# Optimization experiments

Hardware: AMD Instinct MI355X
Metric: run time of the kernel (lower is better)

Reference implementation:

```python
import jax, jax.numpy as jnp
import numpy as np

V, B, L, NG = 50000, 128, 350, 3        # vocab, batch(docs), doc length, n-gram window
D, H, C = 768, 256, 20                  # bert dim, num_hidden, class_num
HEADS, LAYERS, K, ALPHA = 8, 2, 3, 0.15 # GAT heads/layers, diffusion hops k, alpha


def setup_inputs() -> dict:
    rng = np.random.default_rng(0)
    # per-doc graphs: 350 unique word-ids per doc (nodes), n-gram window edges
    node_ids = np.stack([rng.choice(V, L, replace=False) for _ in range(B)]).ravel()
    src_b, dst_b = [], []
    for i in range(L):
        for j in range(max(0, i - NG), min(L, i + NG + 1)):
            src_b.append(i); dst_b.append(j)
    src_b, dst_b = np.asarray(src_b), np.asarray(dst_b)
    off = (np.arange(B) * L)[:, None]
    edge_src = (src_b[None, :] + off).ravel()
    edge_dst = (dst_b[None, :] + off).ravel()
    graph_id = np.repeat(np.arange(B), L)

    ks = jax.random.split(jax.random.key(0), 8)
    f32 = jnp.float32
    return {
        'node_ids': jnp.asarray(node_ids, jnp.int32),
        'edge_src': jnp.asarray(edge_src, jnp.int32),
        'edge_dst': jnp.asarray(edge_dst, jnp.int32),
        'graph_id': jnp.asarray(graph_id, jnp.int32),
        'emb':    (jax.random.normal(ks[0], (V, D), f32) * 0.02),
        'W1':     (jax.random.normal(ks[1], (D, H), f32) / np.sqrt(D)).astype(f32),
        'b1':     jnp.zeros((H,), f32),
        'W2':     (jax.random.normal(ks[2], (H, C), f32) / np.sqrt(H)).astype(f32),
        'b2':     jnp.zeros((C,), f32),
        'gat_W':  (jax.random.normal(ks[3], (LAYERS, HEADS, C, C), f32) / np.sqrt(C)).astype(f32),
        'a_src':  (jax.random.normal(ks[4], (LAYERS, HEADS, C), f32) * 0.1),
        'a_dst':  (jax.random.normal(ks[5], (LAYERS, HEADS, C), f32) * 0.1),
        'w_gate': (jax.random.normal(ks[6], (C,), f32) / np.sqrt(C)).astype(f32),
        'b_gate': jnp.zeros((), f32),
    }


def _gat_layer(h, W, a_s, a_d, src, dst, N):
    # h: [N,C]; W: [Hd,C,C]; a_s/a_d: [Hd,C]
    z = jnp.einsum('nc,hcd->hnd', h, W)                     # [Hd,N,C]
    e = jax.nn.leaky_relu(jnp.einsum('hnd,hd->hn', z, a_s)[:, src]
                          + jnp.einsum('hnd,hd->hn', z, a_d)[:, dst], 0.2)  # [Hd,E]

    def segsoftmax(ev):  # edge softmax over incoming edges at each dst node
        m = jax.ops.segment_max(ev, dst, num_segments=N)
        ex = jnp.exp(ev - m[dst])
        s = jax.ops.segment_sum(ex, dst, num_segments=N)
        return ex / (s[dst] + 1e-9)

    att = jax.vmap(segsoftmax)(e)                           # [Hd,E]

    def diffuse(zh, ah):  # attention diffusion: Z_t = (1-a) A Z_{t-1} + a Z_0
        zt = zh
        for _ in range(K):
            agg = jax.ops.segment_sum(ah[:, None] * zt[src], dst, num_segments=N)
            zt = (1.0 - ALPHA) * agg + ALPHA * zh
        return zt

    out = jax.vmap(diffuse)(z, att)                         # [Hd,N,C]
    return jax.nn.elu(out).mean(axis=0)                     # merge='mean'


def reference(node_ids, edge_src, edge_dst, graph_id, emb, W1, b1, W2, b2,
              gat_W, a_src, a_dst, w_gate, b_gate):
    N = node_ids.shape[0]
    x = emb[node_ids]                                       # [N,768] gather
    x = jax.nn.relu(x @ W1 + b1)                            # linear1 + ReLU
    h = x @ W2 + b2                                         # linear2 -> [N,C]
    for l in range(LAYERS):
        h = _gat_layer(h, gat_W[l], a_src[l], a_dst[l], edge_src, edge_dst, N)
    gate = jax.nn.sigmoid(h @ w_gate + b_gate)[:, None]     # WeightAndSum gate
    return jax.ops.segment_sum(gate * h, graph_id, num_segments=B)  # [B,C]
```

## Files before the change

kernel.cpp:

```cpp
#include <hip/hip_runtime.h>
#include <hip/hip_bf16.h>
#include <cstddef>

#define NB_NODES 44800
#define NDOCS 128
#define DLEN 350
#define DIM 768
#define HID 256
#define NCLS 20
#define NHEADS 8
#define ZSTR 24

typedef __bf16 v8bf __attribute__((ext_vector_type(8)));
typedef __bf16 v4bf __attribute__((ext_vector_type(4)));
typedef float v4f __attribute__((ext_vector_type(4)));

__global__ __launch_bounds__(256) void k_transpose(const float* __restrict__ W1,
                                                   __bf16* __restrict__ W1T) {
  int idx = blockIdx.x * 256 + threadIdx.x;
  int n = idx / 768, k = idx - n * 768;
  W1T[idx] = (__bf16)W1[k * 256 + n];
}

__global__ __launch_bounds__(256) void k_mlp(
    const int* __restrict__ node_ids, const float* __restrict__ emb,
    const __bf16* __restrict__ W1T, const float* __restrict__ b1,
    const float* __restrict__ W2, const float* __restrict__ b2,
    float* __restrict__ h0) {
  __shared__ __align__(16) char smem[43520];
  __bf16* As = (__bf16*)smem;
  float*  xs = (float*)smem;
  __bf16* w2s = (__bf16*)(smem + 33280);
  int tid = threadIdx.x;
  int wave = tid >> 6, lane = tid & 63;
  int quad = lane >> 4, l16 = lane & 15;
  int m0 = blockIdx.x * 64;

  int lrow = tid & 15;
  int lk4  = (tid >> 4) & 3;
  int khalf = (tid >> 6) & 1;
  int msubA = tid >> 7;
  int kbase = khalf * 32 + lk4 * 8;
  const float* apA = emb + (size_t)node_ids[m0 + msubA * 16 + lrow] * DIM + kbase;
  const float* apB = emb + (size_t)node_ids[m0 + (msubA + 2) * 16 + lrow] * DIM + kbase;

  v4f acc[4][4];
#pragma unroll
  for (int ms = 0; ms < 4; ++ms)
#pragma unroll
    for (int j = 0; j < 4; ++j) acc[ms][j] = (v4f){0.f, 0.f, 0.f, 0.f};

  v4f pf[4];
  pf[0] = *(const v4f*)(apA); pf[1] = *(const v4f*)(apA + 4);
  pf[2] = *(const v4f*)(apB); pf[3] = *(const v4f*)(apB + 4);

  for (int kc = 0; kc < 12; ++kc) {
    __bf16* buf = As + (kc & 1) * 4096;
    v8bf w0, w1;
#pragma unroll
    for (int e = 0; e < 4; ++e) {
      w0[e] = (__bf16)pf[0][e]; w0[4 + e] = (__bf16)pf[1][e];
      w1[e] = (__bf16)pf[2][e]; w1[4 + e] = (__bf16)pf[3][e];
    }
    *(v8bf*)(buf + tid * 8) = w0;
    *(v8bf*)(buf + tid * 8 + 2048) = w1;
    if (kc < 11) {
      int k1 = (kc + 1) * 64;
      pf[0] = *(const v4f*)(apA + k1); pf[1] = *(const v4f*)(apA + k1 + 4);
      pf[2] = *(const v4f*)(apB + k1); pf[3] = *(const v4f*)(apB + k1 + 4);
    }
    __syncthreads();

#pragma unroll
    for (int ks = 0; ks < 2; ++ks) {
      v8bf af[4], bv[4];
#pragma unroll
      for (int ms = 0; ms < 4; ++ms)
        af[ms] = *(const v8bf*)(buf + ((ms * 2 + ks) * 64 + lane) * 8);
#pragma unroll
      for (int j = 0; j < 4; ++j)
        bv[j] = *(const v8bf*)(W1T + (size_t)(wave * 64 + j * 16 + l16) * DIM + kc * 64 + ks * 32 + quad * 8);
#pragma unroll
      for (int ms = 0; ms < 4; ++ms)
#pragma unroll
        for (int j = 0; j < 4; ++j)
          acc[ms][j] = __builtin_amdgcn_mfma_f32_16x16x32_bf16(af[ms], bv[j], acc[ms][j], 0, 0, 0);
    }
  }

  __syncthreads();
  for (int i = tid; i < HID * NCLS; i += 256) w2s[i] = (__bf16)W2[i];

#pragma unroll
  for (int p = 0; p < 2; ++p) {
    if (p) __syncthreads();
#pragma unroll
    for (int mh = 0; mh < 2; ++mh) {
      int ms = p * 2 + mh;
#pragma unroll
      for (int j = 0; j < 4; ++j) {
        int col = wave * 64 + j * 16 + l16;
        float bb = b1[col];
#pragma unroll
        for (int r = 0; r < 4; ++r) {
          int lr = mh * 16 + quad * 4 + r;
          float v = acc[ms][j][r] + bb;
          xs[lr * 260 + col] = v > 0.f ? v : 0.f;
        }
      }
    }
    __syncthreads();
    if (tid < 160) {
      int m = tid / 5, c0 = (tid % 5) * 4;
      v4f s = *(const v4f*)(b2 + c0);
      for (int k = 0; k < HID; ++k) {
        float x = xs[m * 260 + k];
        v4bf w = *(const v4bf*)(w2s + k * NCLS + c0);
        s[0] += x * (float)w[0]; s[1] += x * (float)w[1];
        s[2] += x * (float)w[2]; s[3] += x * (float)w[3];
      }
      *(v4f*)(h0 + (size_t)(m0 + p * 32 + m) * NCLS + c0) = s;
    }
  }
}

__global__ __launch_bounds__(384) void k_gat(
    const float* __restrict__ hin, const float* __restrict__ gatW,
    const float* __restrict__ a_src, const float* __restrict__ a_dst,
    int layer, float* __restrict__ zout) {
  __shared__ float zA[DLEN * ZSTR];
  __shared__ float asv[DLEN], adv[DLEN];
  int tid = threadIdx.x;
  int head = blockIdx.x & 7;
  int doc = blockIdx.x >> 3;
  const float* W  = gatW  + (size_t)(layer * NHEADS + head) * NCLS * NCLS;
  const float* av = a_src + (layer * NHEADS + head) * NCLS;
  const float* dv = a_dst + (layer * NHEADS + head) * NCLS;
  int r = tid;
  bool act = r < DLEN;

  float z0[NCLS];
  if (act) {
    const float* hr = hin + ((size_t)doc * DLEN + r) * NCLS;
    float h[NCLS];
#pragma unroll
    for (int q = 0; q < 5; ++q) {
      v4f t = *(const v4f*)(hr + q * 4);
#pragma unroll
      for (int e = 0; e < 4; ++e) h[q * 4 + e] = t[e];
    }
    float zacc[NCLS];
#pragma unroll
    for (int d = 0; d < NCLS; ++d) zacc[d] = 0.f;
#pragma unroll
    for (int c = 0; c < NCLS; ++c) {
      float hc = h[c];
#pragma unroll
      for (int d = 0; d < NCLS; ++d) zacc[d] += hc * W[c * NCLS + d];
    }
    float sa = 0.f, sd = 0.f;
#pragma unroll
    for (int d = 0; d < NCLS; ++d) { sa += zacc[d] * av[d]; sd += zacc[d] * dv[d]; }
    asv[r] = sa; adv[r] = sd;
#pragma unroll
    for (int q = 0; q < 5; ++q) {
      v4f t;
#pragma unroll
      for (int e = 0; e < 4; ++e) t[e] = zacc[q * 4 + e];
      *(v4f*)(zA + r * ZSTR + q * 4) = t;
    }
#pragma unroll
    for (int d = 0; d < NCLS; ++d) z0[d] = zacc[d];
  }
  __syncthreads();

  float att[7];
  if (act) {
    float ad = adv[r];
    float e[7]; float m = -1e30f;
#pragma unroll
    for (int j = 0; j < 7; ++j) {
      int s = r - 3 + j;
      bool valid = (s >= 0) && (s < DLEN);
      float x = valid ? asv[s] + ad : -1e30f;
      x = x > 0.f ? x : 0.2f * x;
      e[j] = valid ? x : -1e30f;
      if (e[j] > m) m = e[j];
    }
    float sum = 0.f;
#pragma unroll
    for (int j = 0; j < 7; ++j) {
      float ex = (e[j] > -1e29f) ? expf(e[j] - m) : 0.f;
      e[j] = ex; sum += ex;
    }
    float inv = 1.f / (sum + 1e-9f);
#pragma unroll
    for (int j = 0; j < 7; ++j) att[j] = e[j] * inv;
  }

  float vn[NCLS];
  for (int hop = 0; hop < 3; ++hop) {
    if (act) {
      v4f agg[5];
#pragma unroll
      for (int q = 0; q < 5; ++q) agg[q] = (v4f){0.f, 0.f, 0.f, 0.f};
#pragma unroll
      for (int j = 0; j < 7; ++j) {
        int s = r - 3 + j;
        s = s < 0 ? 0 : (s > DLEN - 1 ? DLEN - 1 : s);
        float a = att[j];
#pragma unroll
        for (int q = 0; q < 5; ++q) {
          v4f zq = *(const v4f*)(zA + s * ZSTR + q * 4);
#pragma unroll
          for (int e = 0; e < 4; ++e) agg[q][e] += a * zq[e];
        }
      }
#pragma unroll
      for (int q = 0; q < 5; ++q)
#pragma unroll
        for (int e = 0; e < 4; ++e)
          vn[q * 4 + e] = 0.85f * agg[q][e] + 0.15f * z0[q * 4 + e];
    }
    if (hop < 2) {
      __syncthreads();
      if (act) {
#pragma unroll
        for (int q = 0; q < 5; ++q) {
          v4f t;
#pragma unroll
          for (int e = 0; e < 4; ++e) t[e] = vn[q * 4 + e];
          *(v4f*)(zA + r * ZSTR + q * 4) = t;
        }
      }
      __syncthreads();
    }
  }

  if (act) {
    float* og = zout + ((size_t)head * NB_NODES + (size_t)doc * DLEN + r) * NCLS;
#pragma unroll
    for (int q = 0; q < 5; ++q) {
      v4f t;
#pragma unroll
      for (int e = 0; e < 4; ++e) {
        float x = vn[q * 4 + e];
        t[e] = x > 0.f ? x : expf(x) - 1.f;
      }
      *(v4f*)(og + q * 4) = t;
    }
  }
}

__global__ __launch_bounds__(256) void k_headmean(
    const float* __restrict__ eluzt, float* __restrict__ hout) {
  int idx = blockIdx.x * 256 + threadIdx.x;
  v4f s = (v4f){0.f, 0.f, 0.f, 0.f};
#pragma unroll
  for (int h = 0; h < NHEADS; ++h)
    s += ((const v4f*)eluzt)[(size_t)h * (NB_NODES * NCLS / 4) + idx];
  v4f o; o[0] = s[0] * 0.125f; o[1] = s[1] * 0.125f; o[2] = s[2] * 0.125f; o[3] = s[3] * 0.125f;
  ((v4f*)hout)[idx] = o;
}

__global__ __launch_bounds__(64) void k_pool(
    const float* __restrict__ hfin, const float* __restrict__ w_gate,
    const float* __restrict__ b_gate, float* __restrict__ out) {
  int b = blockIdx.x, lane = threadIdx.x;
  float wg[NCLS];
#pragma unroll
  for (int c = 0; c < NCLS; ++c) wg[c] = w_gate[c];
  float bg = b_gate[0];
  float acc[NCLS];
#pragma unroll
  for (int c = 0; c < NCLS; ++c) acc[c] = 0.f;
  for (int n = lane; n < DLEN; n += 64) {
    const v4f* hr = (const v4f*)(hfin + ((size_t)b * DLEN + n) * NCLS);
    float hv[NCLS];
    float d = bg;
#pragma unroll
    for (int q = 0; q < 5; ++q) {
      v4f t = hr[q];
#pragma unroll
      for (int j = 0; j < 4; ++j) { hv[q * 4 + j] = t[j]; d += t[j] * wg[q * 4 + j]; }
    }
    float g = 1.f / (1.f + expf(-d));
#pragma unroll
    for (int c = 0; c < NCLS; ++c) acc[c] += g * hv[c];
  }
#pragma unroll
  for (int off = 32; off > 0; off >>= 1)
#pragma unroll
    for (int c = 0; c < NCLS; ++c) acc[c] += __shfl_down(acc[c], off);
  if (lane == 0)
#pragma unroll
    for (int c = 0; c < NCLS; ++c) out[b * NCLS + c] = acc[c];
}

extern "C" void kernel_launch(void* const* d_in, const int* in_sizes, int n_in,
                              void* d_out, int out_size, void* d_ws, size_t ws_size,
                              hipStream_t stream) {
  const int* node_ids = (const int*)d_in[0];
  const float* emb    = (const float*)d_in[4];
  const float* W1     = (const float*)d_in[5];
  const float* b1     = (const float*)d_in[6];
  const float* W2     = (const float*)d_in[7];
  const float* b2     = (const float*)d_in[8];
  const float* gatW   = (const float*)d_in[9];
  const float* a_src  = (const float*)d_in[10];
  const float* a_dst  = (const float*)d_in[11];
  const float* w_gate = (const float*)d_in[12];
  const float* b_gate = (const float*)d_in[13];
  float* out = (float*)d_out;
  char* ws = (char*)d_ws;

  __bf16* W1T = (__bf16*)(ws + 0);
  float* hA  = (float*)(ws + 393216);
  float* hB  = (float*)(ws + 3977216);
  float* zt  = (float*)(ws + 7561216);

  k_transpose<<<768, 256, 0, stream>>>(W1, W1T);
  k_mlp<<<NB_NODES / 64, 256, 0, stream>>>(node_ids, emb, W1T, b1, W2, b2, hA);
  k_gat<<<NDOCS * NHEADS, 384, 0, stream>>>(hA, gatW, a_src, a_dst, 0, zt);
  k_headmean<<<(NB_NODES * NCLS / 4) / 256, 256, 0, stream>>>(zt, hB);
  k_gat<<<NDOCS * NHEADS, 384, 0, stream>>>(hB, gatW, a_src, a_dst, 1, zt);
  k_headmean<<<(NB_NODES * NCLS / 4) / 256, 256, 0, stream>>>(zt, hA);
  k_pool<<<NDOCS, 64, 0, stream>>>(hA, w_gate, b_gate, out);
}
```

Before: 361.7 us.

## Tile W1 transpose, hoist W1T loads, read W2 directly, shrink LDS strides

The W1 transpose now goes through a 32x33 shared-memory tile, so both its global reads and writes are coalesced, and it launches 192 blocks. In the MLP kernel, all B-fragment loads for a k-chunk are issued before the MFMA loop to overlap latency, and the bf16 W2 staging in LDS is dropped in favour of direct fp32 global reads, which shrinks LDS use and may raise occupancy. The xs row stride changes from 260 to 258 and the GAT z stride from 24 to 20, which may change bank conflicts or alignment for the vector loads. Dropping the bf16 copy of W2 also changes precision slightly, and hoisting the loads raises register pressure.

```diff
diff --git a/kernel.cpp b/kernel.cpp
--- a/kernel.cpp
+++ b/kernel.cpp
@@ -9,17 +9,25 @@
 #define HID 256
 #define NCLS 20
 #define NHEADS 8
-#define ZSTR 24
+#define ZSTR 20
 
 typedef __bf16 v8bf __attribute__((ext_vector_type(8)));
-typedef __bf16 v4bf __attribute__((ext_vector_type(4)));
 typedef float v4f __attribute__((ext_vector_type(4)));
 
 __global__ __launch_bounds__(256) void k_transpose(const float* __restrict__ W1,
                                                    __bf16* __restrict__ W1T) {
-  int idx = blockIdx.x * 256 + threadIdx.x;
-  int n = idx / 768, k = idx - n * 768;
-  W1T[idx] = (__bf16)W1[k * 256 + n];
+  __shared__ float tile[32][33];
+  int bx = blockIdx.x % 24;
+  int by = blockIdx.x / 24;
+  int tx = threadIdx.x & 31, ty = threadIdx.x >> 5;
+  int k0 = bx * 32, n0 = by * 32;
+#pragma unroll
+  for (int i = 0; i < 4; ++i)
+    tile[ty + i * 8][tx] = W1[(size_t)(k0 + ty + i * 8) * 256 + n0 + tx];
+  __syncthreads();
+#pragma unroll
+  for (int i = 0; i < 4; ++i)
+    W1T[(size_t)(n0 + ty + i * 8) * 768 + k0 + tx] = (__bf16)tile[tx][ty + i * 8];
 }
 
 __global__ __launch_bounds__(256) void k_mlp(
@@ -27,10 +35,9 @@
     const __bf16* __restrict__ W1T, const float* __restrict__ b1,
     const float* __restrict__ W2, const float* __restrict__ b2,
     float* __restrict__ h0) {
-  __shared__ __align__(16) char smem[43520];
+  __shared__ __align__(16) char smem[33024];
   __bf16* As = (__bf16*)smem;
   float*  xs = (float*)smem;
-  __bf16* w2s = (__bf16*)(smem + 33280);
   int tid = threadIdx.x;
   int wave = tid >> 6, lane = tid & 63;
   int quad = lane >> 4, l16 = lane & 15;
@@ -71,25 +78,27 @@
     }
     __syncthreads();
 
+    v8bf bv[2][4];
+#pragma unroll
+    for (int ks = 0; ks < 2; ++ks)
+#pragma unroll
+      for (int j = 0; j < 4; ++j)
+        bv[ks][j] = *(const v8bf*)(W1T + (size_t)(wave * 64 + j * 16 + l16) * DIM + kc * 64 + ks * 32 + quad * 8);
 #pragma unroll
     for (int ks = 0; ks < 2; ++ks) {
-      v8bf af[4], bv[4];
+      v8bf af[4];
 #pragma unroll
       for (int ms = 0; ms < 4; ++ms)
         af[ms] = *(const v8bf*)(buf + ((ms * 2 + ks) * 64 + lane) * 8);
 #pragma unroll
-      for (int j = 0; j < 4; ++j)
-        bv[j] = *(const v8bf*)(W1T + (size_t)(wave * 64 + j * 16 + l16) * DIM + kc * 64 + ks * 32 + quad * 8);
-#pragma unroll
       for (int ms = 0; ms < 4; ++ms)
 #pragma unroll
         for (int j = 0; j < 4; ++j)
-          acc[ms][j] = __builtin_amdgcn_mfma_f32_16x16x32_bf16(af[ms], bv[j], acc[ms][j], 0, 0, 0);
+          acc[ms][j] = __builtin_amdgcn_mfma_f32_16x16x32_bf16(af[ms], bv[ks][j], acc[ms][j], 0, 0, 0);
     }
   }
 
   __syncthreads();
-  for (int i = tid; i < HID * NCLS; i += 256) w2s[i] = (__bf16)W2[i];
 
 #pragma unroll
   for (int p = 0; p < 2; ++p) {
@@ -105,7 +114,7 @@
         for (int r = 0; r < 4; ++r) {
           int lr = mh * 16 + quad * 4 + r;
           float v = acc[ms][j][r] + bb;
-          xs[lr * 260 + col] = v > 0.f ? v : 0.f;
+          xs[lr * 258 + col] = v > 0.f ? v : 0.f;
         }
       }
     }
@@ -114,10 +123,10 @@
       int m = tid / 5, c0 = (tid % 5) * 4;
       v4f s = *(const v4f*)(b2 + c0);
       for (int k = 0; k < HID; ++k) {
-        float x = xs[m * 260 + k];
-        v4bf w = *(const v4bf*)(w2s + k * NCLS + c0);
-        s[0] += x * (float)w[0]; s[1] += x * (float)w[1];
-        s[2] += x * (float)w[2]; s[3] += x * (float)w[3];
+        float x = xs[m * 258 + k];
+        v4f w = *(const v4f*)(W2 + k * NCLS + c0);
+        s[0] += x * w[0]; s[1] += x * w[1];
+        s[2] += x * w[2]; s[3] += x * w[3];
       }
       *(v4f*)(h0 + (size_t)(m0 + p * 32 + m) * NCLS + c0) = s;
     }
@@ -319,7 +328,7 @@
   float* hB  = (float*)(ws + 3977216);
   float* zt  = (float*)(ws + 7561216);
 
-  k_transpose<<<768, 256, 0, stream>>>(W1, W1T);
+  k_transpose<<<192, 256, 0, stream>>>(W1, W1T);
   k_mlp<<<NB_NODES / 64, 256, 0, stream>>>(node_ids, emb, W1T, b1, W2, b2, hA);
   k_gat<<<NDOCS * NHEADS, 384, 0, stream>>>(hA, gatW, a_src, a_dst, 0, zt);
   k_headmean<<<(NB_NODES * NCLS / 4) / 256, 256, 0, stream>>>(zt, hB);
```

Result: no change. 368.1 us (+1.8%).
